# Kernel optimization log

Measured on AMD Instinct MI355X. Metric: run time of the kernel, lower is better.

The kernel has to match this reference:

```python
import jax, jax.numpy as jnp
import numpy as np

TOPK = 2

def setup_inputs() -> dict:
    key = jax.random.key(0)
    k1, k2, k3, k4 = jax.random.split(key, 4)
    B, L, D, NB = 4, 4096, 1024, 4
    x = jax.random.normal(k1, (B, L, D), dtype=jnp.float32)
    branches = jax.random.normal(k2, (B, L, NB, D), dtype=jnp.float32)  # pre-stacked [B,L,n_branches,D]
    gate_w = jax.random.normal(k3, (D, NB), dtype=jnp.float32) * (1.0 / np.sqrt(D))
    gate_b = jax.random.normal(k4, (NB,), dtype=jnp.float32) * 0.02
    return {"x": x, "branches": branches, "gate_w": gate_w, "gate_b": gate_b}

def reference(x, branches, gate_w, gate_b):
    # gate linear: [B,L,D] @ [D,NB] -> [B,L,NB]
    logits = jnp.einsum("bld,dn->bln", x, gate_w) + gate_b
    nb = logits.shape[-1]
    if TOPK and TOPK < nb:
        vals = jax.lax.top_k(logits, TOPK)[0]          # [B,L,TOPK]
        kth = vals[..., -1:]                            # k-th largest per token
        logits = jnp.where(logits >= kth, logits, -jnp.inf)
    w = jax.nn.softmax(logits, axis=-1)                 # [B,L,NB]
    # weighted branch combine: sum_n w[...,n] * branches[...,n,:]
    fused = jnp.einsum("bln,blnd->bld", w, branches)
    return fused
```

## Files before the change

### kernel.cpp

```cpp
#include <hip/hip_runtime.h>
#include <hip/hip_bf16.h>
#include <math.h>


#define DDIM 1024
#define NBR 4

__global__ __launch_bounds__(256) void titan_fuse_kernel(
    const float* __restrict__ x,
    const float* __restrict__ branches,
    const float* __restrict__ gate_w,
    const float* __restrict__ gate_b,
    float* __restrict__ out,
    int nrows)
{
    const int lane = threadIdx.x & 63;
    const int wave = threadIdx.x >> 6;
    const int waves_per_block = blockDim.x >> 6;
    const int total_waves = gridDim.x * waves_per_block;
    const int wave_id = blockIdx.x * waves_per_block + wave;

    float4 gw[4][4];
#pragma unroll
    for (int j = 0; j < 4; ++j)
#pragma unroll
        for (int k = 0; k < 4; ++k)
            gw[j][k] = *(const float4*)(gate_w + (size_t)((j * 256 + lane * 4 + k) * NBR));

    const float4 gb = *(const float4*)gate_b;

    for (int row = wave_id; row < nrows; row += total_waves) {
        const float* xr = x + (size_t)row * DDIM;

        float acc0 = 0.f, acc1 = 0.f, acc2 = 0.f, acc3 = 0.f;
#pragma unroll
        for (int j = 0; j < 4; ++j) {
            const float4 xv = *(const float4*)(xr + j * 256 + lane * 4);
            const float xs[4] = {xv.x, xv.y, xv.z, xv.w};
#pragma unroll
            for (int k = 0; k < 4; ++k) {
                acc0 = fmaf(xs[k], gw[j][k].x, acc0);
                acc1 = fmaf(xs[k], gw[j][k].y, acc1);
                acc2 = fmaf(xs[k], gw[j][k].z, acc2);
                acc3 = fmaf(xs[k], gw[j][k].w, acc3);
            }
        }
#pragma unroll
        for (int off = 32; off >= 1; off >>= 1) {
            acc0 += __shfl_xor(acc0, off, 64);
            acc1 += __shfl_xor(acc1, off, 64);
            acc2 += __shfl_xor(acc2, off, 64);
            acc3 += __shfl_xor(acc3, off, 64);
        }

        float lg[NBR] = {acc0 + gb.x, acc1 + gb.y, acc2 + gb.z, acc3 + gb.w};

        float m1 = -INFINITY, m2 = -INFINITY;
#pragma unroll
        for (int n = 0; n < NBR; ++n) {
            const float v = lg[n];
            if (v > m1) { m2 = m1; m1 = v; }
            else if (v > m2) { m2 = v; }
        }

        float w[NBR];
        float s = 0.f;
#pragma unroll
        for (int n = 0; n < NBR; ++n) {
            const float e = (lg[n] >= m2) ? expf(lg[n] - m1) : 0.0f;
            w[n] = e;
            s += e;
        }
        const float inv = 1.0f / s;
#pragma unroll
        for (int n = 0; n < NBR; ++n) w[n] *= inv;

        const float* br = branches + (size_t)row * (NBR * DDIM);
        float* outr = out + (size_t)row * DDIM;
#pragma unroll
        for (int j = 0; j < 4; ++j) {
            const int d = j * 256 + lane * 4;
            const float4 b0 = *(const float4*)(br + 0 * DDIM + d);
            const float4 b1 = *(const float4*)(br + 1 * DDIM + d);
            const float4 b2 = *(const float4*)(br + 2 * DDIM + d);
            const float4 b3 = *(const float4*)(br + 3 * DDIM + d);
            float4 o;
            o.x = w[0] * b0.x + w[1] * b1.x + w[2] * b2.x + w[3] * b3.x;
            o.y = w[0] * b0.y + w[1] * b1.y + w[2] * b2.y + w[3] * b3.y;
            o.z = w[0] * b0.z + w[1] * b1.z + w[2] * b2.z + w[3] * b3.z;
            o.w = w[0] * b0.w + w[1] * b1.w + w[2] * b2.w + w[3] * b3.w;
            *(float4*)(outr + d) = o;
        }
    }
}

extern "C" void kernel_launch(void* const* d_in, const int* in_sizes, int n_in,
                              void* d_out, int out_size, void* d_ws, size_t ws_size,
                              hipStream_t stream) {
    const float* x        = (const float*)d_in[0];
    const float* branches = (const float*)d_in[1];
    const float* gate_w   = (const float*)d_in[2];
    const float* gate_b   = (const float*)d_in[3];
    float* out = (float*)d_out;

    const int nrows = in_sizes[0] / DDIM;

    const int block = 256;
    const int grid = 2048;
    hipLaunchKernelGGL(titan_fuse_kernel, dim3(grid), dim3(block), 0, stream,
                       x, branches, gate_w, gate_b, out, nrows);
}
```

Baseline: 82.93 us.

## Split gating and branch blending into two kernels using workspace weights

Replaces the single fused kernel with a gate kernel, which writes per-row softmax weights to the workspace, followed by a blend kernel that streams the branches. Each kernel launches one wave per row. The gate kernel also swaps the four separate butterfly reductions for a transpose-style shuffle reduction with fewer shuffles. The split aims to shrink register pressure in the bandwidth-heavy blend pass and raise occupancy. The cost is a second launch, a small workspace round trip, and losing overlap of x reads with branch reads. The old fused kernel remains as a fallback when no workspace is available.

```diff
diff --git a/kernel.cpp b/kernel.cpp
--- a/kernel.cpp
+++ b/kernel.cpp
@@ -6,7 +6,123 @@
 #define DDIM 1024
 #define NBR 4
 
-__global__ __launch_bounds__(256) void titan_fuse_kernel(
+__global__ __launch_bounds__(256) void gate_kernel(
+    const float* __restrict__ x,
+    const float* __restrict__ gate_w,
+    const float* __restrict__ gate_b,
+    float* __restrict__ wout,
+    int nrows)
+{
+    const int lane = threadIdx.x & 63;
+    const int wave = threadIdx.x >> 6;
+    const int waves_per_block = blockDim.x >> 6;
+    const int total_waves = gridDim.x * waves_per_block;
+    const int wave_id = blockIdx.x * waves_per_block + wave;
+
+    float4 gw[4][4];
+#pragma unroll
+    for (int j = 0; j < 4; ++j)
+#pragma unroll
+        for (int k = 0; k < 4; ++k)
+            gw[j][k] = *(const float4*)(gate_w + (size_t)((j * 256 + lane * 4 + k) * NBR));
+
+    const float4 gb = *(const float4*)gate_b;
+
+    for (int row = wave_id; row < nrows; row += total_waves) {
+        const float* xr = x + (size_t)row * DDIM;
+
+        float a0 = 0.f, a1 = 0.f, a2 = 0.f, a3 = 0.f;
+#pragma unroll
+        for (int j = 0; j < 4; ++j) {
+            const float4 xv = *(const float4*)(xr + j * 256 + lane * 4);
+            const float xs[4] = {xv.x, xv.y, xv.z, xv.w};
+#pragma unroll
+            for (int k = 0; k < 4; ++k) {
+                a0 = fmaf(xs[k], gw[j][k].x, a0);
+                a1 = fmaf(xs[k], gw[j][k].y, a1);
+                a2 = fmaf(xs[k], gw[j][k].z, a2);
+                a3 = fmaf(xs[k], gw[j][k].w, a3);
+            }
+        }
+
+        const bool keep1 = (lane & 1) == 0;
+        float u0 = keep1 ? a0 : a2;
+        float u1 = keep1 ? a1 : a3;
+        float s0 = keep1 ? a2 : a0;
+        float s1 = keep1 ? a3 : a1;
+        u0 += __shfl_xor(s0, 1, 64);
+        u1 += __shfl_xor(s1, 1, 64);
+        const bool keep2 = (lane & 2) == 0;
+        float v = keep2 ? u0 : u1;
+        float s = keep2 ? u1 : u0;
+        v += __shfl_xor(s, 2, 64);
+#pragma unroll
+        for (int off = 4; off <= 32; off <<= 1)
+            v += __shfl_xor(v, off, 64);
+        const float t1 = __shfl_xor(v, 1, 64);
+        const float t2 = __shfl_xor(v, 2, 64);
+        const float t3 = __shfl_xor(v, 3, 64);
+
+        float lg[NBR] = {v + gb.x, t2 + gb.y, t1 + gb.z, t3 + gb.w};
+
+        float m1 = -INFINITY, m2 = -INFINITY;
+#pragma unroll
+        for (int n = 0; n < NBR; ++n) {
+            const float val = lg[n];
+            if (val > m1) { m2 = m1; m1 = val; }
+            else if (val > m2) { m2 = val; }
+        }
+        float w[NBR];
+        float sum = 0.f;
+#pragma unroll
+        for (int n = 0; n < NBR; ++n) {
+            const float e = (lg[n] >= m2) ? expf(lg[n] - m1) : 0.0f;
+            w[n] = e;
+            sum += e;
+        }
+        const float inv = 1.0f / sum;
+
+        if (lane == 0) {
+            float4 wv = make_float4(w[0] * inv, w[1] * inv, w[2] * inv, w[3] * inv);
+            *(float4*)(wout + (size_t)row * NBR) = wv;
+        }
+    }
+}
+
+__global__ __launch_bounds__(256) void blend_kernel(
+    const float* __restrict__ branches,
+    const float* __restrict__ wrow,
+    float* __restrict__ out,
+    int nrows)
+{
+    const int lane = threadIdx.x & 63;
+    const int wave = threadIdx.x >> 6;
+    const int waves_per_block = blockDim.x >> 6;
+    const int total_waves = gridDim.x * waves_per_block;
+    const int wave_id = blockIdx.x * waves_per_block + wave;
+
+    for (int row = wave_id; row < nrows; row += total_waves) {
+        const float4 w = *(const float4*)(wrow + (size_t)row * NBR);
+        const float* br = branches + (size_t)row * (NBR * DDIM);
+        float* outr = out + (size_t)row * DDIM;
+#pragma unroll
+        for (int j = 0; j < 4; ++j) {
+            const int d = j * 256 + lane * 4;
+            const float4 b0 = *(const float4*)(br + 0 * DDIM + d);
+            const float4 b1 = *(const float4*)(br + 1 * DDIM + d);
+            const float4 b2 = *(const float4*)(br + 2 * DDIM + d);
+            const float4 b3 = *(const float4*)(br + 3 * DDIM + d);
+            float4 o;
+            o.x = w.x * b0.x + w.y * b1.x + w.z * b2.x + w.w * b3.x;
+            o.y = w.x * b0.y + w.y * b1.y + w.z * b2.y + w.w * b3.y;
+            o.z = w.x * b0.z + w.y * b1.z + w.z * b2.z + w.w * b3.z;
+            o.w = w.x * b0.w + w.y * b1.w + w.z * b2.w + w.w * b3.w;
+            *(float4*)(outr + d) = o;
+        }
+    }
+}
+
+__global__ __launch_bounds__(256) void titan_fused_kernel(
     const float* __restrict__ x,
     const float* __restrict__ branches,
     const float* __restrict__ gate_w,
@@ -26,52 +142,45 @@
 #pragma unroll
         for (int k = 0; k < 4; ++k)
             gw[j][k] = *(const float4*)(gate_w + (size_t)((j * 256 + lane * 4 + k) * NBR));
-
     const float4 gb = *(const float4*)gate_b;
 
     for (int row = wave_id; row < nrows; row += total_waves) {
         const float* xr = x + (size_t)row * DDIM;
-
-        float acc0 = 0.f, acc1 = 0.f, acc2 = 0.f, acc3 = 0.f;
+        float a0 = 0.f, a1 = 0.f, a2 = 0.f, a3 = 0.f;
 #pragma unroll
         for (int j = 0; j < 4; ++j) {
             const float4 xv = *(const float4*)(xr + j * 256 + lane * 4);
             const float xs[4] = {xv.x, xv.y, xv.z, xv.w};
 #pragma unroll
             for (int k = 0; k < 4; ++k) {
-                acc0 = fmaf(xs[k], gw[j][k].x, acc0);
-                acc1 = fmaf(xs[k], gw[j][k].y, acc1);
-                acc2 = fmaf(xs[k], gw[j][k].z, acc2);
-                acc3 = fmaf(xs[k], gw[j][k].w, acc3);
+                a0 = fmaf(xs[k], gw[j][k].x, a0);
+                a1 = fmaf(xs[k], gw[j][k].y, a1);
+                a2 = fmaf(xs[k], gw[j][k].z, a2);
+                a3 = fmaf(xs[k], gw[j][k].w, a3);
             }
         }
 #pragma unroll
         for (int off = 32; off >= 1; off >>= 1) {
-            acc0 += __shfl_xor(acc0, off, 64);
-            acc1 += __shfl_xor(acc1, off, 64);
-            acc2 += __shfl_xor(acc2, off, 64);
-            acc3 += __shfl_xor(acc3, off, 64);
-        }
-
-        float lg[NBR] = {acc0 + gb.x, acc1 + gb.y, acc2 + gb.z, acc3 + gb.w};
-
+            a0 += __shfl_xor(a0, off, 64);
+            a1 += __shfl_xor(a1, off, 64);
+            a2 += __shfl_xor(a2, off, 64);
+            a3 += __shfl_xor(a3, off, 64);
+        }
+        float lg[NBR] = {a0 + gb.x, a1 + gb.y, a2 + gb.z, a3 + gb.w};
         float m1 = -INFINITY, m2 = -INFINITY;
 #pragma unroll
         for (int n = 0; n < NBR; ++n) {
-            const float v = lg[n];
-            if (v > m1) { m2 = m1; m1 = v; }
-            else if (v > m2) { m2 = v; }
-        }
-
-        float w[NBR];
-        float s = 0.f;
+            const float val = lg[n];
+            if (val > m1) { m2 = m1; m1 = val; }
+            else if (val > m2) { m2 = val; }
+        }
+        float w[NBR]; float sum = 0.f;
 #pragma unroll
         for (int n = 0; n < NBR; ++n) {
             const float e = (lg[n] >= m2) ? expf(lg[n] - m1) : 0.0f;
-            w[n] = e;
-            s += e;
-        }
-        const float inv = 1.0f / s;
+            w[n] = e; sum += e;
+        }
+        const float inv = 1.0f / sum;
 #pragma unroll
         for (int n = 0; n < NBR; ++n) w[n] *= inv;
 
@@ -104,9 +213,18 @@
     float* out = (float*)d_out;
 
     const int nrows = in_sizes[0] / DDIM;
-
-    const int block = 256;
-    const int grid = 2048;
-    hipLaunchKernelGGL(titan_fuse_kernel, dim3(grid), dim3(block), 0, stream,
-                       x, branches, gate_w, gate_b, out, nrows);
-}
+    const size_t need_ws = (size_t)nrows * NBR * sizeof(float);
+
+    if (d_ws != nullptr && ws_size >= need_ws) {
+        float* wrow = (float*)d_ws;
+        const int blocks1 = (nrows + 3) / 4;
+        hipLaunchKernelGGL(gate_kernel, dim3(blocks1), dim3(256), 0, stream,
+                           x, gate_w, gate_b, wrow, nrows);
+        const int blocks2 = (nrows + 3) / 4;
+        hipLaunchKernelGGL(blend_kernel, dim3(blocks2), dim3(256), 0, stream,
+                           branches, wrow, out, nrows);
+    } else {
+        hipLaunchKernelGGL(titan_fused_kernel, dim3(2048), dim3(256), 0, stream,
+                           x, branches, gate_w, gate_b, out, nrows);
+    }
+}
```

After: 90.14 us. 1.09x slower.
